# Kernel tuning notes

Hardware: AMD Instinct MI355X
Metric: run time of the kernel (lower is better)

## Reference

```python
import jax, jax.numpy as jnp
import numpy as np


def sparsemax(z):
    # z: [..., E] -> sparse probability simplex projection (Martins & Astudillo 2016).
    E = z.shape[-1]
    z_sorted = -jnp.sort(-z, axis=-1)                 # descending
    z_cum = jnp.cumsum(z_sorted, axis=-1)
    k = jnp.arange(1, E + 1, dtype=z.dtype)
    support = (1.0 + k * z_sorted) > z_cum            # [..., E] bool
    k_z = jnp.sum(support, axis=-1, keepdims=True)    # support size >= 1
    tau_sum = jnp.take_along_axis(z_cum, k_z.astype(jnp.int32) - 1, axis=-1)
    tau = (tau_sum - 1.0) / k_z.astype(z.dtype)
    return jnp.maximum(z - tau, 0.0)


def setup_inputs() -> dict:
    key = jax.random.key(0)
    ks = jax.random.split(key, 6)
    B, S, D_IN, D_OUT, E, R = 8, 2048, 4096, 4096, 8, 16
    x = jax.random.normal(ks[0], (B, S, D_IN), dtype=jnp.float32)
    W_base = jax.random.normal(ks[1], (D_OUT, D_IN), dtype=jnp.float32) * (D_IN ** -0.5)
    b_base = jax.random.normal(ks[2], (D_OUT,), dtype=jnp.float32) * 0.01
    W_router = jax.random.normal(ks[3], (E, D_IN), dtype=jnp.float32) * (D_IN ** -0.5)
    b_router = jnp.zeros((E,), dtype=jnp.float32)
    lora_A = jax.random.normal(ks[4], (E, D_IN, R), dtype=jnp.float32) * (D_IN ** -0.5)
    lora_B = jnp.zeros((E, R, D_OUT), dtype=jnp.float32)  # standard LoRA zero-init on B
    return {"x": x, "W_base": W_base, "b_base": b_base,
            "W_router": W_router, "b_router": b_router,
            "lora_A": lora_A, "lora_B": lora_B}


def reference(x, W_base, b_base, W_router, b_router, lora_A, lora_B):
    # Frozen base projection: [B,S,D_in] @ [D_in,D_out]
    base_out = jnp.einsum('bsd,od->bso', x, W_base) + b_base
    # Sparsegen (sparsemax) router over experts
    logits = jnp.einsum('bsd,ed->bse', x, W_router) + b_router
    weights = sparsemax(logits)                       # [B,S,E], mostly-sparse
    # LoRA experts: low-rank path per expert, summed with token-dependent weights
    h = jnp.einsum('bsd,edr->bser', x, lora_A)        # [B,S,E,R]
    expert_out = jnp.einsum('bser,bse,ero->bso', h, weights, lora_B)
    return base_out + expert_out
```

## Files before the change

kernel.cpp:

```cpp
#include <hip/hip_runtime.h>
#include <hip/hip_bf16.h>

#define M_TOK 16384
#define DK    4096
#define DN    4096
#define NE    8
#define NR    16
#define ERC   128
#define RAC   160
#define NT_MAIN 128
#define NT_ALL  132

typedef __attribute__((ext_vector_type(8))) short bfrag;
typedef __attribute__((ext_vector_type(4))) float f32x4;

__device__ __forceinline__ unsigned short f2bf(float f) {
  unsigned u = __builtin_bit_cast(unsigned, f);
  unsigned rounding = 0x7FFFu + ((u >> 16) & 1u);
  u += rounding;
  return (unsigned short)(u >> 16);
}

__device__ __forceinline__ void load_lds16(const void* g, void* l) {
  __builtin_amdgcn_global_load_lds(
      (__attribute__((address_space(1))) void*)(g),
      (__attribute__((address_space(3))) void*)(l), 16, 0, 0);
}

__global__ void k_cvt(const float* __restrict__ in, unsigned short* __restrict__ out, long n4) {
  long i = (long)blockIdx.x * blockDim.x + threadIdx.x;
  long stride = (long)gridDim.x * blockDim.x;
  for (; i < n4; i += stride) {
    float4 v = reinterpret_cast<const float4*>(in)[i];
    ushort4 o;
    o.x = f2bf(v.x); o.y = f2bf(v.y); o.z = f2bf(v.z); o.w = f2bf(v.w);
    reinterpret_cast<ushort4*>(out)[i] = o;
  }
}

__global__ void k_build_ra(const float* __restrict__ Wr, const float* __restrict__ lA,
                           unsigned short* __restrict__ RA) {
  int idx = blockIdx.x * 256 + threadIdx.x;
  if (idx >= RAC * DK) return;
  int c = idx >> 12;
  int k = idx & (DK - 1);
  float v = 0.f;
  if (c < NE) {
    v = Wr[c * DK + k];
  } else if (c < NE + ERC) {
    int er = c - NE;
    int e = er >> 4, r = er & 15;
    v = lA[((long)e * DK + k) * NR + r];
  }
  RA[idx] = f2bf(v);
}

__global__ void k_build_bt(const float* __restrict__ lB, unsigned short* __restrict__ BT) {
  int idx = blockIdx.x * 256 + threadIdx.x;
  if (idx >= DN * ERC) return;
  int n = idx >> 7;
  int kp = idx & 127;
  BT[idx] = f2bf(lB[(long)kp * DN + n]);
}

__global__ __launch_bounds__(256, 2)
void k_gemm_small(const unsigned short* __restrict__ X, const unsigned short* __restrict__ RA,
                  float* __restrict__ H) {
  __shared__ unsigned short At[64 * 64];
  __shared__ unsigned short Bt[RAC * 64];
  int m0 = blockIdx.x * 64;
  int tid = threadIdx.x;
  int lane = tid & 63, wid = tid >> 6;
  int wr = wid >> 1, wc = wid & 1;
  int l16 = lane & 15, lhi = lane >> 4;
  f32x4 acc[2][5] = {};
  int byteoff = tid * 16;
  for (int k0 = 0; k0 < DK; k0 += 64) {
#pragma unroll
    for (int r = 0; r < 2; r++) {
      int off = r * 4096 + byteoff;
      int row = off >> 7, colb = off & 127;
      load_lds16((const char*)X + ((long)(m0 + row) * DK + k0) * 2 + colb, (char*)At + off);
    }
#pragma unroll
    for (int r = 0; r < 5; r++) {
      int off = r * 4096 + byteoff;
      int row = off >> 7, colb = off & 127;
      load_lds16((const char*)RA + ((long)row * DK + k0) * 2 + colb, (char*)Bt + off);
    }
    __syncthreads();
#pragma unroll
    for (int kk = 0; kk < 2; kk++) {
      bfrag a[2], b[5];
#pragma unroll
      for (int m = 0; m < 2; m++)
        a[m] = *(const bfrag*)&At[(wr * 32 + m * 16 + l16) * 64 + kk * 32 + lhi * 8];
#pragma unroll
      for (int n = 0; n < 5; n++)
        b[n] = *(const bfrag*)&Bt[(wc * 80 + n * 16 + l16) * 64 + kk * 32 + lhi * 8];
#pragma unroll
      for (int m = 0; m < 2; m++)
#pragma unroll
        for (int n = 0; n < 5; n++)
          acc[m][n] = __builtin_amdgcn_mfma_f32_16x16x32_bf16(a[m], b[n], acc[m][n], 0, 0, 0);
    }
    __syncthreads();
  }
#pragma unroll
  for (int m = 0; m < 2; m++)
#pragma unroll
    for (int n = 0; n < 5; n++) {
      int col = wc * 80 + n * 16 + l16;
      int row = m0 + wr * 32 + m * 16 + lhi * 4;
#pragma unroll
      for (int j = 0; j < 4; j++)
        H[(long)(row + j) * RAC + col] = acc[m][n][j];
    }
}

__global__ void k_router(const float* __restrict__ H, const float* __restrict__ b_router,
                         unsigned short* __restrict__ G) {
  int t = blockIdx.x * blockDim.x + threadIdx.x;
  if (t >= M_TOK) return;
  const float* row = H + (long)t * RAC;
  float z[NE], zs[NE];
#pragma unroll
  for (int e = 0; e < NE; e++) { z[e] = row[e] + b_router[e]; zs[e] = z[e]; }
#pragma unroll
  for (int i = 1; i < NE; i++) {
    float key = zs[i];
    int j = i - 1;
    while (j >= 0 && zs[j] < key) { zs[j + 1] = zs[j]; j--; }
    zs[j + 1] = key;
  }
  float cums[NE];
  float cum = 0.f;
#pragma unroll
  for (int j = 0; j < NE; j++) { cum += zs[j]; cums[j] = cum; }
  int kz = 0;
#pragma unroll
  for (int j = 0; j < NE; j++)
    if (1.f + (float)(j + 1) * zs[j] > cums[j]) kz = j + 1;
  float tau = (cums[kz - 1] - 1.f) / (float)kz;
#pragma unroll
  for (int e = 0; e < NE; e++) {
    float we = fmaxf(z[e] - tau, 0.f);
#pragma unroll
    for (int r = 0; r < NR; r++)
      G[(long)t * ERC + e * NR + r] = f2bf(we * row[NE + e * NR + r]);
  }
}

struct KtArgs {
  const unsigned short *pXA0, *pXA1, *pWB0, *pWB1, *pGA0, *pGA1, *pTB0, *pTB1;
  int soffA0, soffA1, soffB0, soffB1;
  int wr, wc, l16, swslot;
};

template<int VMW, bool ISSUE>
__device__ __forceinline__ void ktile_body(int t, unsigned short* lds, const KtArgs& A,
                                           f32x4 (&acc)[8][4]) {
  if constexpr (VMW == 8)      asm volatile("s_waitcnt vmcnt(8)\n\ts_barrier" ::: "memory");
  else if constexpr (VMW == 4) asm volatile("s_waitcnt vmcnt(4)\n\ts_barrier" ::: "memory");
  else                         asm volatile("s_waitcnt vmcnt(0)\n\ts_barrier" ::: "memory");

  unsigned short* s = lds + (t & 3) * 16384;
  if (ISSUE) {
    int u = t + 3;
    unsigned short* d = lds + (u & 3) * 16384;
    if (u < NT_MAIN) {
      load_lds16(A.pXA0 + (long)u * 32, d + A.soffA0);
      load_lds16(A.pXA1 + (long)u * 32, d + A.soffA1);
    } else {
      load_lds16(A.pGA0 + (long)(u - NT_MAIN) * 32, d + A.soffA0);
      load_lds16(A.pGA1 + (long)(u - NT_MAIN) * 32, d + A.soffA1);
    }
  }
  bfrag bfr[4], afr[4];
#pragma unroll
  for (int n = 0; n < 4; n++)
    bfr[n] = *(const bfrag*)&s[8192 + (A.wc * 64 + n * 16 + A.l16) * 32 + A.swslot];
#pragma unroll
  for (int m = 0; m < 4; m++)
    afr[m] = *(const bfrag*)&s[(A.wr * 128 + m * 16 + A.l16) * 32 + A.swslot];
  __builtin_amdgcn_s_setprio(1);
#pragma unroll
  for (int m = 0; m < 4; m++)
#pragma unroll
    for (int n = 0; n < 4; n++)
      acc[m][n] = __builtin_amdgcn_mfma_f32_16x16x32_bf16(afr[m], bfr[n], acc[m][n], 0, 0, 0);
  __builtin_amdgcn_s_setprio(0);
  asm volatile("s_barrier" ::: "memory");
  if (ISSUE) {
    int u = t + 3;
    unsigned short* d = lds + (u & 3) * 16384;
    if (u < NT_MAIN) {
      load_lds16(A.pWB0 + (long)u * 32, d + A.soffB0);
      load_lds16(A.pWB1 + (long)u * 32, d + A.soffB1);
    } else {
      load_lds16(A.pTB0 + (long)(u - NT_MAIN) * 32, d + A.soffB0);
      load_lds16(A.pTB1 + (long)(u - NT_MAIN) * 32, d + A.soffB1);
    }
  }
#pragma unroll
  for (int m = 0; m < 4; m++)
    afr[m] = *(const bfrag*)&s[(A.wr * 128 + 64 + m * 16 + A.l16) * 32 + A.swslot];
  __builtin_amdgcn_s_setprio(1);
#pragma unroll
  for (int m = 0; m < 4; m++)
#pragma unroll
    for (int n = 0; n < 4; n++)
      acc[4 + m][n] = __builtin_amdgcn_mfma_f32_16x16x32_bf16(afr[m], bfr[n], acc[4 + m][n], 0, 0, 0);
  __builtin_amdgcn_s_setprio(0);
}

__global__ __launch_bounds__(512, 2)
void k_gemm_main(const unsigned short* __restrict__ X, const unsigned short* __restrict__ W,
                 const unsigned short* __restrict__ G, const unsigned short* __restrict__ BT,
                 const float* __restrict__ bias, float* __restrict__ out) {
  __shared__ unsigned short lds[4 * 16384];
  int bid = blockIdx.x;
  int swz = (bid & 7) * 128 + (bid >> 3);
  int bm = swz >> 4, bn = swz & 15;
  int m0 = bm * 256, n0 = bn * 256;
  int tid = threadIdx.x;
  int lane = tid & 63, wid = tid >> 6;

  KtArgs A;
  A.wr = wid >> 2; A.wc = wid & 3;
  A.l16 = lane & 15;
  int lhi = lane >> 4;
  A.swslot = (lhi ^ ((A.l16 >> 1) & 3)) * 8;
  int r0 = tid >> 2;
  int c8 = (((tid & 3) ^ ((tid >> 3) & 3)) * 8);
  A.pXA0 = X + (long)(m0 + r0) * DK + c8;
  A.pXA1 = X + (long)(m0 + 128 + r0) * DK + c8;
  A.pWB0 = W + (long)(n0 + r0) * DK + c8;
  A.pWB1 = W + (long)(n0 + 128 + r0) * DK + c8;
  A.pGA0 = G + (long)(m0 + r0) * ERC + c8;
  A.pGA1 = G + (long)(m0 + 128 + r0) * ERC + c8;
  A.pTB0 = BT + (long)(n0 + r0) * ERC + c8;
  A.pTB1 = BT + (long)(n0 + 128 + r0) * ERC + c8;
  A.soffA0 = tid * 8;
  A.soffA1 = 4096 + tid * 8;
  A.soffB0 = 8192 + tid * 8;
  A.soffB1 = 12288 + tid * 8;

  f32x4 acc[8][4] = {};

#pragma unroll
  for (int u = 0; u < 3; u++) {
    unsigned short* d = lds + u * 16384;
    load_lds16(A.pXA0 + (long)u * 32, d + A.soffA0);
    load_lds16(A.pXA1 + (long)u * 32, d + A.soffA1);
    load_lds16(A.pWB0 + (long)u * 32, d + A.soffB0);
    load_lds16(A.pWB1 + (long)u * 32, d + A.soffB1);
  }

  for (int t = 0; t <= NT_ALL - 4; t++)
    ktile_body<8, true>(t, lds, A, acc);
  ktile_body<8, false>(NT_ALL - 3, lds, A, acc);
  ktile_body<4, false>(NT_ALL - 2, lds, A, acc);
  ktile_body<0, false>(NT_ALL - 1, lds, A, acc);

  int lhi2 = lane >> 4;
#pragma unroll
  for (int n = 0; n < 4; n++) {
    int col = n0 + A.wc * 64 + n * 16 + A.l16;
    float bv = bias[col];
#pragma unroll
    for (int m = 0; m < 8; m++) {
      int row = m0 + A.wr * 128 + m * 16 + lhi2 * 4;
#pragma unroll
      for (int j = 0; j < 4; j++)
        out[(long)(row + j) * DN + col] = acc[m][n][j] + bv;
    }
  }
}

extern "C" void kernel_launch(void* const* d_in, const int* in_sizes, int n_in,
                              void* d_out, int out_size, void* d_ws, size_t ws_size,
                              hipStream_t stream) {
  const float* x        = (const float*)d_in[0];
  const float* W_base   = (const float*)d_in[1];
  const float* b_base   = (const float*)d_in[2];
  const float* W_router = (const float*)d_in[3];
  const float* b_router = (const float*)d_in[4];
  const float* lora_A   = (const float*)d_in[5];
  const float* lora_B   = (const float*)d_in[6];
  float* out = (float*)d_out;

  char* ws = (char*)d_ws;
  unsigned short* Xb = (unsigned short*)ws;
  unsigned short* Wb = (unsigned short*)(ws + 134217728L);
  unsigned short* RA = (unsigned short*)(ws + 167772160L);
  unsigned short* BT = (unsigned short*)(ws + 169082880L);
  float*          H  = (float*)(ws + 170131456L);
  unsigned short* G  = (unsigned short*)(ws + 180617216L);

  hipLaunchKernelGGL(k_cvt, dim3(2048), dim3(256), 0, stream, x, Xb, (long)M_TOK * DK / 4);
  hipLaunchKernelGGL(k_cvt, dim3(2048), dim3(256), 0, stream, W_base, Wb, (long)DN * DK / 4);
  hipLaunchKernelGGL(k_build_ra, dim3((RAC * DK + 255) / 256), dim3(256), 0, stream,
                     W_router, lora_A, RA);
  hipLaunchKernelGGL(k_build_bt, dim3((DN * ERC + 255) / 256), dim3(256), 0, stream, lora_B, BT);
  hipLaunchKernelGGL(k_gemm_small, dim3(M_TOK / 64), dim3(256), 0, stream, Xb, RA, H);
  hipLaunchKernelGGL(k_router, dim3(M_TOK / 256), dim3(256), 0, stream, H, b_router, G);
  hipLaunchKernelGGL(k_gemm_main, dim3((M_TOK / 256) * (DN / 256)), dim3(512), 0, stream,
                     Xb, Wb, G, BT, b_base, out);
}
```

Measured before the change: 714.4 us.

## Prefetch next k-tile fragments into registers and use one barrier per tile

Restructures the GEMM main loop so each k-tile needs a single waitcnt plus barrier instead of two. All four global-to-LDS loads for a future tile are issued together. The A/B fragments of the next tile are read from LDS into a second register set while the current tile's MFMAs run, which overlaps LDS reads with MFMA work and cuts synchronisation. The cost is extra fragment registers under a 512-thread, 2-block launch bound, which could cause spills or lower occupancy.

```diff
diff --git a/kernel.cpp b/kernel.cpp
--- a/kernel.cpp
+++ b/kernel.cpp
@@ -157,60 +157,58 @@
   int wr, wc, l16, swslot;
 };
 
-template<int VMW, bool ISSUE>
+template<int VMW, bool STAGE, bool READF>
 __device__ __forceinline__ void ktile_body(int t, unsigned short* lds, const KtArgs& A,
-                                           f32x4 (&acc)[8][4]) {
-  if constexpr (VMW == 8)      asm volatile("s_waitcnt vmcnt(8)\n\ts_barrier" ::: "memory");
-  else if constexpr (VMW == 4) asm volatile("s_waitcnt vmcnt(4)\n\ts_barrier" ::: "memory");
-  else                         asm volatile("s_waitcnt vmcnt(0)\n\ts_barrier" ::: "memory");
-
-  unsigned short* s = lds + (t & 3) * 16384;
-  if (ISSUE) {
+                                           f32x4 (&acc)[8][4],
+                                           bfrag (&bc)[4], bfrag (&ac)[4],
+                                           bfrag (&bn)[4], bfrag (&an)[4]) {
+  if constexpr (VMW == 4) asm volatile("s_waitcnt vmcnt(4)\n\ts_barrier" ::: "memory");
+  else                    asm volatile("s_waitcnt vmcnt(0)\n\ts_barrier" ::: "memory");
+
+  if constexpr (STAGE) {
     int u = t + 3;
     unsigned short* d = lds + (u & 3) * 16384;
     if (u < NT_MAIN) {
       load_lds16(A.pXA0 + (long)u * 32, d + A.soffA0);
       load_lds16(A.pXA1 + (long)u * 32, d + A.soffA1);
-    } else {
-      load_lds16(A.pGA0 + (long)(u - NT_MAIN) * 32, d + A.soffA0);
-      load_lds16(A.pGA1 + (long)(u - NT_MAIN) * 32, d + A.soffA1);
-    }
-  }
-  bfrag bfr[4], afr[4];
-#pragma unroll
-  for (int n = 0; n < 4; n++)
-    bfr[n] = *(const bfrag*)&s[8192 + (A.wc * 64 + n * 16 + A.l16) * 32 + A.swslot];
-#pragma unroll
-  for (int m = 0; m < 4; m++)
-    afr[m] = *(const bfrag*)&s[(A.wr * 128 + m * 16 + A.l16) * 32 + A.swslot];
-  __builtin_amdgcn_s_setprio(1);
-#pragma unroll
-  for (int m = 0; m < 4; m++)
-#pragma unroll
-    for (int n = 0; n < 4; n++)
-      acc[m][n] = __builtin_amdgcn_mfma_f32_16x16x32_bf16(afr[m], bfr[n], acc[m][n], 0, 0, 0);
-  __builtin_amdgcn_s_setprio(0);
-  asm volatile("s_barrier" ::: "memory");
-  if (ISSUE) {
-    int u = t + 3;
-    unsigned short* d = lds + (u & 3) * 16384;
-    if (u < NT_MAIN) {
       load_lds16(A.pWB0 + (long)u * 32, d + A.soffB0);
       load_lds16(A.pWB1 + (long)u * 32, d + A.soffB1);
     } else {
-      load_lds16(A.pTB0 + (long)(u - NT_MAIN) * 32, d + A.soffB0);
-      load_lds16(A.pTB1 + (long)(u - NT_MAIN) * 32, d + A.soffB1);
-    }
-  }
+      long v = u - NT_MAIN;
+      load_lds16(A.pGA0 + v * 32, d + A.soffA0);
+      load_lds16(A.pGA1 + v * 32, d + A.soffA1);
+      load_lds16(A.pTB0 + v * 32, d + A.soffB0);
+      load_lds16(A.pTB1 + v * 32, d + A.soffB1);
+    }
+  }
+
+  unsigned short* s = lds + (t & 3) * 16384;
+  bfrag ah[4];
 #pragma unroll
   for (int m = 0; m < 4; m++)
-    afr[m] = *(const bfrag*)&s[(A.wr * 128 + 64 + m * 16 + A.l16) * 32 + A.swslot];
+    ah[m] = *(const bfrag*)&s[(A.wr * 128 + 64 + m * 16 + A.l16) * 32 + A.swslot];
+  if constexpr (READF) {
+    unsigned short* sn = lds + ((t + 1) & 3) * 16384;
+#pragma unroll
+    for (int n = 0; n < 4; n++)
+      bn[n] = *(const bfrag*)&sn[8192 + (A.wc * 64 + n * 16 + A.l16) * 32 + A.swslot];
+#pragma unroll
+    for (int m = 0; m < 4; m++)
+      an[m] = *(const bfrag*)&sn[(A.wr * 128 + m * 16 + A.l16) * 32 + A.swslot];
+  }
   __builtin_amdgcn_s_setprio(1);
 #pragma unroll
   for (int m = 0; m < 4; m++)
 #pragma unroll
     for (int n = 0; n < 4; n++)
-      acc[4 + m][n] = __builtin_amdgcn_mfma_f32_16x16x32_bf16(afr[m], bfr[n], acc[4 + m][n], 0, 0, 0);
+      acc[m][n] = __builtin_amdgcn_mfma_f32_16x16x32_bf16(ac[m], bc[n], acc[m][n], 0, 0, 0);
+  __builtin_amdgcn_s_setprio(0);
+  __builtin_amdgcn_s_setprio(1);
+#pragma unroll
+  for (int m = 0; m < 4; m++)
+#pragma unroll
+    for (int n = 0; n < 4; n++)
+      acc[4 + m][n] = __builtin_amdgcn_mfma_f32_16x16x32_bf16(ah[m], bc[n], acc[4 + m][n], 0, 0, 0);
   __builtin_amdgcn_s_setprio(0);
 }
 
@@ -256,21 +254,31 @@
     load_lds16(A.pWB0 + (long)u * 32, d + A.soffB0);
     load_lds16(A.pWB1 + (long)u * 32, d + A.soffB1);
   }
-
-  for (int t = 0; t <= NT_ALL - 4; t++)
-    ktile_body<8, true>(t, lds, A, acc);
-  ktile_body<8, false>(NT_ALL - 3, lds, A, acc);
-  ktile_body<4, false>(NT_ALL - 2, lds, A, acc);
-  ktile_body<0, false>(NT_ALL - 1, lds, A, acc);
-
-  int lhi2 = lane >> 4;
+  asm volatile("s_waitcnt vmcnt(8)\n\ts_barrier" ::: "memory");
+  bfrag b0[4], a0[4], b1[4], a1[4];
+#pragma unroll
+  for (int n = 0; n < 4; n++)
+    b0[n] = *(const bfrag*)&lds[8192 + (A.wc * 64 + n * 16 + A.l16) * 32 + A.swslot];
+#pragma unroll
+  for (int m = 0; m < 4; m++)
+    a0[m] = *(const bfrag*)&lds[(A.wr * 128 + m * 16 + A.l16) * 32 + A.swslot];
+
+  for (int tt = 0; tt < 128; tt += 2) {
+    ktile_body<4, true, true>(tt,     lds, A, acc, b0, a0, b1, a1);
+    ktile_body<4, true, true>(tt + 1, lds, A, acc, b1, a1, b0, a0);
+  }
+  ktile_body<4, true,  true >(128, lds, A, acc, b0, a0, b1, a1);
+  ktile_body<4, false, true >(129, lds, A, acc, b1, a1, b0, a0);
+  ktile_body<0, false, true >(130, lds, A, acc, b0, a0, b1, a1);
+  ktile_body<0, false, false>(131, lds, A, acc, b1, a1, b0, a0);
+
 #pragma unroll
   for (int n = 0; n < 4; n++) {
     int col = n0 + A.wc * 64 + n * 16 + A.l16;
     float bv = bias[col];
 #pragma unroll
     for (int m = 0; m < 8; m++) {
-      int row = m0 + A.wr * 128 + m * 16 + lhi2 * 4;
+      int row = m0 + A.wr * 128 + m * 16 + lhi * 4;
 #pragma unroll
       for (int j = 0; j < 4; j++)
         out[(long)(row + j) * DN + col] = acc[m][n][j] + bv;
```

Result: slower. 894.9 us (+25.3%).
